# Performance work log

Hardware: AMD Instinct MI355X
Metric: run time of the kernel (lower is better)

## Reference

```python
import jax, jax.numpy as jnp
import numpy as np

NEG_SLOPE = 0.2

def gat_conv(x, src, dst, n, W, a_src, a_dst, b):
    # PyG GATConv, heads=1: h = xW; e_ij = LeakyReLU(a_src.h_j + a_dst.h_i)
    # alpha = softmax over incoming edges of i; out_i = sum_j alpha_ij * h_j + b
    h = x @ W                               # [N, F_out]
    s_src = h @ a_src                       # [N]
    s_dst = h @ a_dst                       # [N]
    e = s_src[src] + s_dst[dst]             # [E]
    e = jnp.where(e > 0, e, NEG_SLOPE * e)  # leaky relu
    # numerically stable scatter-softmax over destination groups
    m = jax.ops.segment_max(e, dst, num_segments=n)          # [N]
    ee = jnp.exp(e - m[dst])                                  # [E]
    denom = jax.ops.segment_sum(ee, dst, num_segments=n)      # [N]
    alpha = ee / denom[dst]                                    # [E]
    out = jax.ops.segment_sum(alpha[:, None] * h[src], dst, num_segments=n)
    return out + b

def add_self_loops(edge_index, n):
    loops = jnp.arange(n, dtype=edge_index.dtype)
    src = jnp.concatenate([edge_index[0], loops])
    dst = jnp.concatenate([edge_index[1], loops])
    return src, dst

def setup_inputs() -> dict:
    key = jax.random.key(0)
    ks = jax.random.split(key, 12)
    N, E, F_IN, H1, H2, C = 50000, 800000, 1433, 512, 256, 7
    x = jax.random.normal(ks[0], (N, F_IN), dtype=jnp.float32)
    edge_index = jax.random.randint(ks[1], (2, E), 0, N, dtype=jnp.int64)
    def glorot(k, shape):
        lim = float(np.sqrt(6.0 / (shape[0] + shape[-1])))
        return jax.random.uniform(k, shape, jnp.float32, -lim, lim)
    params = {
        'W1': glorot(ks[2], (F_IN, H1)), 'as1': glorot(ks[3], (H1,)), 'ad1': glorot(ks[4], (H1,)), 'b1': jnp.zeros((H1,), jnp.float32),
        'W2': glorot(ks[5], (H1, H2)), 'as2': glorot(ks[6], (H2,)), 'ad2': glorot(ks[7], (H2,)), 'b2': jnp.zeros((H2,), jnp.float32),
        'W3': glorot(ks[8], (H2, C)), 'as3': glorot(ks[9], (C,)), 'ad3': glorot(ks[10], (C,)), 'b3': jnp.zeros((C,), jnp.float32),
    }
    return {'x': x, 'edge_index': edge_index, **params}

def reference(x, edge_index, W1, as1, ad1, b1, W2, as2, ad2, b2, W3, as3, ad3, b3):
    n = x.shape[0]
    src, dst = add_self_loops(edge_index, n)
    h = jax.nn.relu(gat_conv(x, src, dst, n, W1, as1, ad1, b1))
    h = jax.nn.relu(gat_conv(h, src, dst, n, W2, as2, ad2, b2))
    h = gat_conv(h, src, dst, n, W3, as3, ad3, b3)
    return jax.nn.log_softmax(h, axis=1)
```

## Files before the change

### kernel.cpp

```cpp
#include <hip/hip_runtime.h>
#include <hip/hip_bf16.h>
#include <math.h>

constexpr int N_NODES = 50000;
constexpr int E_EDGES = 800000;
constexpr int E_TOT   = E_EDGES + N_NODES;
constexpr int F_IN  = 1433;
constexpr int KPAD1 = 1440;
constexpr int F1 = 512;
constexpr int F2 = 256;
constexpr int NC = 7;
constexpr int MAXDEG = 1024;
constexpr float NEG_SLOPE = 0.2f;

typedef unsigned short u16;
typedef unsigned int   u32;
typedef short s16x8 __attribute__((ext_vector_type(8)));
typedef u32   u32x4 __attribute__((ext_vector_type(4)));
typedef float f32x4 __attribute__((ext_vector_type(4)));

__device__ inline u16 f2b(float f) {
    u32 u = __float_as_uint(f);
    u32 r = (u + 0x7fffu + ((u >> 16) & 1u)) >> 16;
    return (u16)r;
}
__device__ inline float b2f(u16 b) { return __uint_as_float(((u32)b) << 16); }

__device__ inline u32 pkbf16(float lo, float hi) {
    union { __hip_bfloat162 h; u32 u; } c;
    c.h = __float22bfloat162_rn(make_float2(lo, hi));
    return c.u;
}

__device__ inline void gload_lds16(const void* g, void* l) {
    __builtin_amdgcn_global_load_lds(
        (const __attribute__((address_space(1))) u32*)g,
        (__attribute__((address_space(3))) u32*)l, 16, 0, 0);
}

__global__ void count_dst_kernel(const int* __restrict__ dst, int* __restrict__ counts) {
    int i = blockIdx.x * blockDim.x + threadIdx.x;
    if (i < E_TOT) {
        int d = (i < E_EDGES) ? dst[i] : (i - E_EDGES);
        atomicAdd(&counts[d], 1);
    }
}

__global__ __launch_bounds__(1024) void scan_kernel(const int* __restrict__ counts,
                                                    int* __restrict__ row_ptr, int n) {
    __shared__ int part[1024];
    int t = threadIdx.x;
    int chunk = (n + 1023) / 1024;
    int lo = t * chunk;
    int hi = min(lo + chunk, n);
    int s = 0;
    for (int i = lo; i < hi; ++i) s += counts[i];
    part[t] = s;
    __syncthreads();
    for (int off = 1; off < 1024; off <<= 1) {
        int v = 0;
        if (t >= off) v = part[t - off];
        __syncthreads();
        part[t] += v;
        __syncthreads();
    }
    int run = part[t] - s;
    for (int i = lo; i < hi; ++i) { row_ptr[i] = run; run += counts[i]; }
    if (t == 1023) row_ptr[n] = part[1023];
}

__global__ void scatter_kernel(const int* __restrict__ src, const int* __restrict__ dst,
                               const int* __restrict__ row_ptr, int* __restrict__ fill,
                               int* __restrict__ col) {
    int i = blockIdx.x * blockDim.x + threadIdx.x;
    if (i < E_TOT) {
        int s = (i < E_EDGES) ? src[i] : (i - E_EDGES);
        int d = (i < E_EDGES) ? dst[i] : (i - E_EDGES);
        int p = row_ptr[d] + atomicAdd(&fill[d], 1);
        col[p] = s;
    }
}

__global__ void convert_wt_kernel(const float* __restrict__ W, u32* __restrict__ Wt,
                                  int K, int Nn, int KP) {
    int p = blockIdx.x * blockDim.x + threadIdx.x;
    int ppr = KP / 2;
    if (p >= Nn * ppr) return;
    int n = p / ppr;
    int k = (p - n * ppr) * 2;
    float v0 = (k + 0 < K) ? W[(size_t)(k + 0) * Nn + n] : 0.f;
    float v1 = (k + 1 < K) ? W[(size_t)(k + 1) * Nn + n] : 0.f;
    Wt[p] = (u32)f2b(v0) | ((u32)f2b(v1) << 16);
}

__global__ __launch_bounds__(256) void mfma_gemm_xf32(const float* __restrict__ A,
                                                      const u16* __restrict__ Bt,
                                                      u16* __restrict__ C,
                                                      int M, int N, int Kf, int K32) {
    __shared__ float sA[128 * 32];
    __shared__ u16  sB[128 * 32];
    int tid  = threadIdx.x;
    int wave = tid >> 6;
    int lane = tid & 63;
    int quad = lane >> 4;
    int lm   = lane & 15;
    int wm = wave & 1;
    int wn = wave >> 1;
    int m0 = blockIdx.y * 128;
    int n0 = blockIdx.x * 128;

    int arow_sub = lane >> 3;
    int acol     = (lane & 7) * 4;
    int brow_sub = lane >> 2;
    int bcol     = (lane & 3) * 8;

    const float* gA[4];
    float* lA[4];
#pragma unroll
    for (int c = 0; c < 4; ++c) {
        int chunk = wave * 4 + c;
        int row = min(m0 + chunk * 8 + arow_sub, M - 1);
        gA[c] = A + (size_t)row * Kf + acol;
        lA[c] = &sA[chunk * 256];
    }
    const u16* gB[2];
    u16* lB[2];
#pragma unroll
    for (int c = 0; c < 2; ++c) {
        int chunk = wave * 2 + c;
        int row = n0 + chunk * 16 + brow_sub;
        gB[c] = Bt + (size_t)row * K32 + bcol;
        lB[c] = &sB[chunk * 512];
    }

    f32x4 acc[4][4];
#pragma unroll
    for (int i = 0; i < 4; ++i)
#pragma unroll
        for (int j = 0; j < 4; ++j) acc[i][j] = (f32x4){0.f, 0.f, 0.f, 0.f};

    int kLast = K32 - 32;
    for (int k0 = 0; k0 <= kLast; k0 += 32) {
        if (k0 < kLast) {
#pragma unroll
            for (int c = 0; c < 4; ++c) gload_lds16(gA[c] + k0, lA[c]);
        } else {
            int colc = min(k0 + acol, Kf - 4);
#pragma unroll
            for (int c = 0; c < 4; ++c) gload_lds16(gA[c] - acol + colc, lA[c]);
        }
#pragma unroll
        for (int c = 0; c < 2; ++c) gload_lds16(gB[c] + k0, lB[c]);
        __syncthreads();

        s16x8 af[4], bf[4];
#pragma unroll
        for (int mt = 0; mt < 4; ++mt) {
            const float* pa = &sA[(wm * 64 + mt * 16 + lm) * 32 + quad * 8];
            float4 u0 = *(const float4*)pa;
            float4 u1 = *(const float4*)(pa + 4);
            u32x4 aw;
            aw[0] = pkbf16(u0.x, u0.y);
            aw[1] = pkbf16(u0.z, u0.w);
            aw[2] = pkbf16(u1.x, u1.y);
            aw[3] = pkbf16(u1.z, u1.w);
            af[mt] = __builtin_bit_cast(s16x8, aw);
        }
#pragma unroll
        for (int nt = 0; nt < 4; ++nt)
            bf[nt] = *(const s16x8*)&sB[(wn * 64 + nt * 16 + lm) * 32 + quad * 8];
#pragma unroll
        for (int mt = 0; mt < 4; ++mt)
#pragma unroll
            for (int nt = 0; nt < 4; ++nt)
                acc[mt][nt] = __builtin_amdgcn_mfma_f32_16x16x32_bf16(
                    af[mt], bf[nt], acc[mt][nt], 0, 0, 0);
        __syncthreads();
    }

#pragma unroll
    for (int mt = 0; mt < 4; ++mt) {
        int mbase = m0 + wm * 64 + mt * 16 + quad * 4;
#pragma unroll
        for (int nt = 0; nt < 4; ++nt) {
            int n = n0 + wn * 64 + nt * 16 + lm;
#pragma unroll
            for (int r = 0; r < 4; ++r) {
                int m = mbase + r;
                if (m < M) C[(size_t)m * N + n] = f2b(acc[mt][nt][r]);
            }
        }
    }
}

__global__ __launch_bounds__(256) void mfma_gemm_bt(const u16* __restrict__ A,
                                                    const u16* __restrict__ Bt,
                                                    u16* __restrict__ C,
                                                    int M, int N, int K) {
    __shared__ u16 sA[128 * 32];
    __shared__ u16 sB[128 * 32];
    int tid  = threadIdx.x;
    int wave = tid >> 6;
    int lane = tid & 63;
    int quad = lane >> 4;
    int lm   = lane & 15;
    int wm = wave & 1;
    int wn = wave >> 1;
    int m0 = blockIdx.y * 128;
    int n0 = blockIdx.x * 128;

    int ch0 = wave * 2, ch1 = wave * 2 + 1;
    int rsub = lane >> 2;
    int csub = (lane & 3) * 8;
    int ar0 = min(m0 + ch0 * 16 + rsub, M - 1);
    int ar1 = min(m0 + ch1 * 16 + rsub, M - 1);
    int br0 = n0 + ch0 * 16 + rsub;
    int br1 = n0 + ch1 * 16 + rsub;
    const u16* gA0 = A + (size_t)ar0 * K + csub;
    const u16* gA1 = A + (size_t)ar1 * K + csub;
    const u16* gB0 = Bt + (size_t)br0 * K + csub;
    const u16* gB1 = Bt + (size_t)br1 * K + csub;

    f32x4 acc[4][4];
#pragma unroll
    for (int i = 0; i < 4; ++i)
#pragma unroll
        for (int j = 0; j < 4; ++j) acc[i][j] = (f32x4){0.f, 0.f, 0.f, 0.f};

    for (int k0 = 0; k0 < K; k0 += 32) {
        gload_lds16(gA0 + k0, &sA[ch0 * 512]);
        gload_lds16(gA1 + k0, &sA[ch1 * 512]);
        gload_lds16(gB0 + k0, &sB[ch0 * 512]);
        gload_lds16(gB1 + k0, &sB[ch1 * 512]);
        __syncthreads();

        s16x8 af[4], bf[4];
#pragma unroll
        for (int mt = 0; mt < 4; ++mt)
            af[mt] = *(const s16x8*)&sA[(wm * 64 + mt * 16 + lm) * 32 + quad * 8];
#pragma unroll
        for (int nt = 0; nt < 4; ++nt)
            bf[nt] = *(const s16x8*)&sB[(wn * 64 + nt * 16 + lm) * 32 + quad * 8];
#pragma unroll
        for (int mt = 0; mt < 4; ++mt)
#pragma unroll
            for (int nt = 0; nt < 4; ++nt)
                acc[mt][nt] = __builtin_amdgcn_mfma_f32_16x16x32_bf16(
                    af[mt], bf[nt], acc[mt][nt], 0, 0, 0);
        __syncthreads();
    }

#pragma unroll
    for (int mt = 0; mt < 4; ++mt) {
        int mbase = m0 + wm * 64 + mt * 16 + quad * 4;
#pragma unroll
        for (int nt = 0; nt < 4; ++nt) {
            int n = n0 + wn * 64 + nt * 16 + lm;
#pragma unroll
            for (int r = 0; r < 4; ++r) {
                int m = mbase + r;
                if (m < M) C[(size_t)m * N + n] = f2b(acc[mt][nt][r]);
            }
        }
    }
}

template <int F>
__global__ __launch_bounds__(256) void scores_bf16_kernel(const u16* __restrict__ h,
                                                          const float* __restrict__ a_src,
                                                          const float* __restrict__ a_dst,
                                                          float* __restrict__ s_src,
                                                          float* __restrict__ s_dst, int n) {
    int gwid = (blockIdx.x * blockDim.x + threadIdx.x) >> 6;
    int lane = threadIdx.x & 63;
    if (gwid >= n) return;
    const u32* row = (const u32*)(h + (size_t)gwid * F);
    float acc1 = 0.f, acc2 = 0.f;
    for (int p = lane; p < F / 2; p += 64) {
        u32 u = row[p];
        float v0 = b2f((u16)(u & 0xffff));
        float v1 = b2f((u16)(u >> 16));
        acc1 += v0 * a_src[2 * p] + v1 * a_src[2 * p + 1];
        acc2 += v0 * a_dst[2 * p] + v1 * a_dst[2 * p + 1];
    }
#pragma unroll
    for (int o = 32; o; o >>= 1) {
        acc1 += __shfl_xor(acc1, o);
        acc2 += __shfl_xor(acc2, o);
    }
    if (lane == 0) { s_src[gwid] = acc1; s_dst[gwid] = acc2; }
}

template <int F>
__global__ __launch_bounds__(256) void scores_kernel(const float* __restrict__ h,
                                                     const float* __restrict__ a_src,
                                                     const float* __restrict__ a_dst,
                                                     float* __restrict__ s_src,
                                                     float* __restrict__ s_dst, int n) {
    int gwid = (blockIdx.x * blockDim.x + threadIdx.x) >> 6;
    int lane = threadIdx.x & 63;
    if (gwid >= n) return;
    const float* row = h + (size_t)gwid * F;
    float acc1 = 0.f, acc2 = 0.f;
    for (int f = lane; f < F; f += 64) {
        float v = row[f];
        acc1 += v * a_src[f];
        acc2 += v * a_dst[f];
    }
#pragma unroll
    for (int o = 32; o; o >>= 1) {
        acc1 += __shfl_xor(acc1, o);
        acc2 += __shfl_xor(acc2, o);
    }
    if (lane == 0) { s_src[gwid] = acc1; s_dst[gwid] = acc2; }
}

template <int F, bool OUT_BF16>
__global__ __launch_bounds__(256) void agg_gather_kernel(const u16* __restrict__ h,
                                                         const float* __restrict__ s_src,
                                                         const float* __restrict__ s_dst,
                                                         const float* __restrict__ bias,
                                                         const int* __restrict__ row_ptr,
                                                         const int* __restrict__ col,
                                                         void* __restrict__ out) {
    constexpr int UPL = F / 128;
    int node = blockIdx.x;
    int tid = threadIdx.x;
    int wave = tid >> 6;
    int lane = tid & 63;
    int beg = row_ptr[node];
    int deg = min(row_ptr[node + 1] - beg, MAXDEG);

    __shared__ float w[MAXDEG];
    __shared__ int cs[MAXDEG];
    __shared__ float sdenom;
    __shared__ float red[4][F];

    if (wave == 0) {
        float sd = s_dst[node];
        float m = -1e30f;
        for (int j = lane; j < deg; j += 64) {
            int s = col[beg + j];
            cs[j] = s;
            float e = s_src[s] + sd;
            e = (e > 0.f) ? e : NEG_SLOPE * e;
            w[j] = e;
            m = fmaxf(m, e);
        }
#pragma unroll
        for (int o = 32; o; o >>= 1) m = fmaxf(m, __shfl_xor(m, o));
        float sum = 0.f;
        for (int j = lane; j < deg; j += 64) {
            float v = expf(w[j] - m);
            w[j] = v;
            sum += v;
        }
#pragma unroll
        for (int o = 32; o; o >>= 1) sum += __shfl_xor(sum, o);
        if (lane == 0) sdenom = sum;
    }
    __syncthreads();
    float inv = 1.0f / sdenom;

    float acc[2 * UPL];
#pragma unroll
    for (int e = 0; e < 2 * UPL; ++e) acc[e] = 0.f;

    int j = wave;
    for (; j + 4 < deg; j += 8) {
        float wg0 = w[j] * inv;
        float wg1 = w[j + 4] * inv;
        const u32* r0 = (const u32*)(h + (size_t)cs[j] * F) + lane * UPL;
        const u32* r1 = (const u32*)(h + (size_t)cs[j + 4] * F) + lane * UPL;
        u32 v0[UPL], v1[UPL];
        if constexpr (UPL == 4) {
            uint4 q0 = *(const uint4*)r0; v0[0] = q0.x; v0[1] = q0.y; v0[2] = q0.z; v0[3] = q0.w;
            uint4 q1 = *(const uint4*)r1; v1[0] = q1.x; v1[1] = q1.y; v1[2] = q1.z; v1[3] = q1.w;
        } else {
            uint2 q0 = *(const uint2*)r0; v0[0] = q0.x; v0[1] = q0.y;
            uint2 q1 = *(const uint2*)r1; v1[0] = q1.x; v1[1] = q1.y;
        }
#pragma unroll
        for (int u = 0; u < UPL; ++u) {
            acc[2 * u]     += wg0 * b2f((u16)(v0[u] & 0xffff)) + wg1 * b2f((u16)(v1[u] & 0xffff));
            acc[2 * u + 1] += wg0 * b2f((u16)(v0[u] >> 16))    + wg1 * b2f((u16)(v1[u] >> 16));
        }
    }
    if (j < deg) {
        float wg = w[j] * inv;
        const u32* r = (const u32*)(h + (size_t)cs[j] * F) + lane * UPL;
        u32 v[UPL];
        if constexpr (UPL == 4) {
            uint4 q = *(const uint4*)r; v[0] = q.x; v[1] = q.y; v[2] = q.z; v[3] = q.w;
        } else {
            uint2 q = *(const uint2*)r; v[0] = q.x; v[1] = q.y;
        }
#pragma unroll
        for (int u = 0; u < UPL; ++u) {
            acc[2 * u]     += wg * b2f((u16)(v[u] & 0xffff));
            acc[2 * u + 1] += wg * b2f((u16)(v[u] >> 16));
        }
    }

#pragma unroll
    for (int e = 0; e < 2 * UPL; ++e) red[wave][lane * 2 * UPL + e] = acc[e];
    __syncthreads();

    if constexpr (OUT_BF16) {
        if (tid < F / 2) {
            int f = tid * 2;
            float v0 = red[0][f] + red[1][f] + red[2][f] + red[3][f] + bias[f];
            float v1 = red[0][f + 1] + red[1][f + 1] + red[2][f + 1] + red[3][f + 1] + bias[f + 1];
            v0 = fmaxf(v0, 0.f);
            v1 = fmaxf(v1, 0.f);
            ((u32*)out)[(size_t)node * (F / 2) + tid] = (u32)f2b(v0) | ((u32)f2b(v1) << 16);
        }
    } else {
        if (tid < F) {
            float v = red[0][tid] + red[1][tid] + red[2][tid] + red[3][tid] + bias[tid];
            ((float*)out)[(size_t)node * F + tid] = fmaxf(v, 0.f);
        }
    }
}

__global__ __launch_bounds__(64) void agg_lsm7_kernel(const float* __restrict__ h,
                                                      const float* __restrict__ s_src,
                                                      const float* __restrict__ s_dst,
                                                      const float* __restrict__ bias,
                                                      const int* __restrict__ row_ptr,
                                                      const int* __restrict__ col,
                                                      float* __restrict__ out) {
    int node = blockIdx.x;
    int lane = threadIdx.x;
    int beg = row_ptr[node];
    int deg = min(row_ptr[node + 1] - beg, MAXDEG);

    __shared__ float w[MAXDEG];
    __shared__ int cs[MAXDEG];

    float sd = s_dst[node];
    float m = -1e30f;
    for (int j = lane; j < deg; j += 64) {
        int s = col[beg + j];
        cs[j] = s;
        float e = s_src[s] + sd;
        e = (e > 0.f) ? e : NEG_SLOPE * e;
        w[j] = e;
        m = fmaxf(m, e);
    }
#pragma unroll
    for (int o = 32; o; o >>= 1) m = fmaxf(m, __shfl_xor(m, o));
    float sum = 0.f;
    for (int j = lane; j < deg; j += 64) {
        float v = expf(w[j] - m);
        w[j] = v;
        sum += v;
    }
#pragma unroll
    for (int o = 32; o; o >>= 1) sum += __shfl_xor(sum, o);
    float inv = 1.0f / sum;

    float a[NC];
#pragma unroll
    for (int f = 0; f < NC; ++f) a[f] = 0.f;
    for (int j = lane; j < deg; j += 64) {
        float wg = w[j] * inv;
        const float* row = h + (size_t)cs[j] * NC;
#pragma unroll
        for (int f = 0; f < NC; ++f) a[f] += wg * row[f];
    }
#pragma unroll
    for (int f = 0; f < NC; ++f)
#pragma unroll
        for (int o = 32; o; o >>= 1) a[f] += __shfl_xor(a[f], o);

    if (lane == 0) {
        float vals[NC];
        float mx = -1e30f;
#pragma unroll
        for (int f = 0; f < NC; ++f) { vals[f] = a[f] + bias[f]; mx = fmaxf(mx, vals[f]); }
        float ssum = 0.f;
#pragma unroll
        for (int f = 0; f < NC; ++f) ssum += expf(vals[f] - mx);
        float lse = mx + logf(ssum);
#pragma unroll
        for (int f = 0; f < NC; ++f) out[(size_t)node * NC + f] = vals[f] - lse;
    }
}

__global__ __launch_bounds__(256) void gemm3_kernel(const float* __restrict__ A,
                                                    const float* __restrict__ W,
                                                    float* __restrict__ out, int n) {
    __shared__ float sW[F2 * NC];
    for (int i = threadIdx.x; i < F2 * NC; i += blockDim.x) sW[i] = W[i];
    __syncthreads();
    int gwid = (blockIdx.x * blockDim.x + threadIdx.x) >> 6;
    int lane = threadIdx.x & 63;
    if (gwid >= n) return;
    const float* row = A + (size_t)gwid * F2;
    float4 v = *(const float4*)(row + lane * 4);
    float res = 0.f;
#pragma unroll
    for (int c = 0; c < NC; ++c) {
        float p = v.x * sW[(lane * 4 + 0) * NC + c] + v.y * sW[(lane * 4 + 1) * NC + c] +
                  v.z * sW[(lane * 4 + 2) * NC + c] + v.w * sW[(lane * 4 + 3) * NC + c];
#pragma unroll
        for (int o = 32; o; o >>= 1) p += __shfl_xor(p, o);
        if (lane == c) res = p;
    }
    if (lane < NC) out[(size_t)gwid * NC + lane] = res;
}

extern "C" void kernel_launch(void* const* d_in, const int* in_sizes, int n_in,
                              void* d_out, int out_size, void* d_ws, size_t ws_size,
                              hipStream_t stream) {
    const float* x   = (const float*)d_in[0];
    const int* ei    = (const int*)d_in[1];
    const int* src   = ei;
    const int* dst   = ei + E_EDGES;
    const float* W1  = (const float*)d_in[2];
    const float* as1 = (const float*)d_in[3];
    const float* ad1 = (const float*)d_in[4];
    const float* b1  = (const float*)d_in[5];
    const float* W2  = (const float*)d_in[6];
    const float* as2 = (const float*)d_in[7];
    const float* ad2 = (const float*)d_in[8];
    const float* b2  = (const float*)d_in[9];
    const float* W3  = (const float*)d_in[10];
    const float* as3 = (const float*)d_in[11];
    const float* ad3 = (const float*)d_in[12];
    const float* b3  = (const float*)d_in[13];
    float* outp = (float*)d_out;

    char* base = (char*)d_ws;
    u16*  a1b = (u16*)base;
    u16*  h2b = (u16*)(base + 51200000);
    float* a2 = (float*)(base + 76800000);
    float* h3 = (float*)(base + 128000000);
    u16*  h1b = (u16*)(base + 144000000);
    u16*  W1t = (u16*)(base + 195200000);
    u16*  W2t = (u16*)(base + 196674560);
    float* ssrc = (float*)(base + 196936704);
    float* sdst = (float*)(base + 197136704);
    int* row_ptr = (int*)(base + 197336704);
    int* counts  = (int*)(base + 197536708);
    int* fill    = (int*)(base + 197736708);
    int* col     = (int*)(base + 197936708);

    hipMemsetAsync(counts, 0, sizeof(int) * N_NODES, stream);
    hipMemsetAsync(fill, 0, sizeof(int) * N_NODES, stream);

    {
        int blk = 256;
        int grid = (E_TOT + blk - 1) / blk;
        count_dst_kernel<<<grid, blk, 0, stream>>>(dst, counts);
        scan_kernel<<<1, 1024, 0, stream>>>(counts, row_ptr, N_NODES);
        scatter_kernel<<<grid, blk, 0, stream>>>(src, dst, row_ptr, fill, col);
    }

    {
        int nw1 = F1 * (KPAD1 / 2);
        convert_wt_kernel<<<(nw1 + 255) / 256, 256, 0, stream>>>(W1, (u32*)W1t, F_IN, F1, KPAD1);
        int nw2 = F2 * (F1 / 2);
        convert_wt_kernel<<<(nw2 + 255) / 256, 256, 0, stream>>>(W2, (u32*)W2t, F1, F2, F1);
    }

    int waves_grid = (N_NODES + 3) / 4;
    int mblocks = (N_NODES + 127) / 128;

    {
        dim3 grid(F1 / 128, mblocks);
        mfma_gemm_xf32<<<grid, 256, 0, stream>>>(x, W1t, h1b, N_NODES, F1, F_IN, KPAD1);
        scores_bf16_kernel<F1><<<waves_grid, 256, 0, stream>>>(h1b, as1, ad1, ssrc, sdst, N_NODES);
        agg_gather_kernel<F1, true><<<N_NODES, 256, 0, stream>>>(
            h1b, ssrc, sdst, b1, row_ptr, col, a1b);
    }
    {
        dim3 grid(F2 / 128, mblocks);
        mfma_gemm_bt<<<grid, 256, 0, stream>>>(a1b, W2t, h2b, N_NODES, F2, F1);
        scores_bf16_kernel<F2><<<waves_grid, 256, 0, stream>>>(h2b, as2, ad2, ssrc, sdst, N_NODES);
        agg_gather_kernel<F2, false><<<N_NODES, 256, 0, stream>>>(
            h2b, ssrc, sdst, b2, row_ptr, col, a2);
    }
    {
        gemm3_kernel<<<waves_grid, 256, 0, stream>>>(a2, W3, h3, N_NODES);
        scores_kernel<NC><<<waves_grid, 256, 0, stream>>>(h3, as3, ad3, ssrc, sdst, N_NODES);
        agg_lsm7_kernel<<<N_NODES, 64, 0, stream>>>(
            h3, ssrc, sdst, b3, row_ptr, col, outp);
    }
}
```

Baseline: 1.117 ms.

## Restructure layer-1 GEMM to 64x512 tiles so x is read once

Layer 1's GEMM now uses 64-row by full-512-column tiles instead of 128x128. Each block reads its rows of fp32 x exactly once, rather than once per each of the four column blocks. The fp32-to-bf16 conversion of A is done once per tile into a separate LDS buffer, not per wave in registers, and the ragged K tail gets its own guarded scalar-load path. This cuts redundant global traffic on the large fp32 input. The cost is 32 accumulators per wave, a much larger B tile in LDS, an extra barrier per K step, and fewer rows per block.

```diff
diff --git a/kernel.cpp b/kernel.cpp
--- a/kernel.cpp
+++ b/kernel.cpp
@@ -16,7 +16,6 @@
 typedef unsigned short u16;
 typedef unsigned int   u32;
 typedef short s16x8 __attribute__((ext_vector_type(8)));
-typedef u32   u32x4 __attribute__((ext_vector_type(4)));
 typedef float f32x4 __attribute__((ext_vector_type(4)));
 
 __device__ inline u16 f2b(float f) {
@@ -93,101 +92,118 @@
     Wt[p] = (u32)f2b(v0) | ((u32)f2b(v1) << 16);
 }
 
-__global__ __launch_bounds__(256) void mfma_gemm_xf32(const float* __restrict__ A,
+__global__ __launch_bounds__(256, 2) void gemm1_fused(const float* __restrict__ A,
                                                       const u16* __restrict__ Bt,
-                                                      u16* __restrict__ C,
-                                                      int M, int N, int Kf, int K32) {
-    __shared__ float sA[128 * 32];
-    __shared__ u16  sB[128 * 32];
+                                                      u16* __restrict__ C) {
+    constexpr int M = N_NODES;
+    __shared__ float sA32[64 * 32];
+    __shared__ u16  sAb[64 * 32];
+    __shared__ u16  sB[512 * 32];
     int tid  = threadIdx.x;
     int wave = tid >> 6;
     int lane = tid & 63;
     int quad = lane >> 4;
     int lm   = lane & 15;
-    int wm = wave & 1;
-    int wn = wave >> 1;
-    int m0 = blockIdx.y * 128;
-    int n0 = blockIdx.x * 128;
-
-    int arow_sub = lane >> 3;
-    int acol     = (lane & 7) * 4;
-    int brow_sub = lane >> 2;
-    int bcol     = (lane & 3) * 8;
-
-    const float* gA[4];
-    float* lA[4];
-#pragma unroll
-    for (int c = 0; c < 4; ++c) {
-        int chunk = wave * 4 + c;
-        int row = min(m0 + chunk * 8 + arow_sub, M - 1);
-        gA[c] = A + (size_t)row * Kf + acol;
-        lA[c] = &sA[chunk * 256];
-    }
-    const u16* gB[2];
-    u16* lB[2];
+    int m0 = blockIdx.x * 64;
+
+    const float* gA[2];
+    float* lA[2];
 #pragma unroll
     for (int c = 0; c < 2; ++c) {
         int chunk = wave * 2 + c;
-        int row = n0 + chunk * 16 + brow_sub;
-        gB[c] = Bt + (size_t)row * K32 + bcol;
+        int row = min(m0 + chunk * 8 + (lane >> 3), M - 1);
+        gA[c] = A + (size_t)row * F_IN + (lane & 7) * 4;
+        lA[c] = &sA32[chunk * 256];
+    }
+    const u16* gB[8];
+    u16* lB[8];
+#pragma unroll
+    for (int c = 0; c < 8; ++c) {
+        int chunk = wave * 8 + c;
+        int row = chunk * 16 + (lane >> 2);
+        gB[c] = Bt + (size_t)row * KPAD1 + (lane & 3) * 8;
         lB[c] = &sB[chunk * 512];
     }
 
-    f32x4 acc[4][4];
+    f32x4 acc[4][8];
 #pragma unroll
     for (int i = 0; i < 4; ++i)
 #pragma unroll
-        for (int j = 0; j < 4; ++j) acc[i][j] = (f32x4){0.f, 0.f, 0.f, 0.f};
-
-    int kLast = K32 - 32;
-    for (int k0 = 0; k0 <= kLast; k0 += 32) {
-        if (k0 < kLast) {
-#pragma unroll
-            for (int c = 0; c < 4; ++c) gload_lds16(gA[c] + k0, lA[c]);
-        } else {
-            int colc = min(k0 + acol, Kf - 4);
-#pragma unroll
-            for (int c = 0; c < 4; ++c) gload_lds16(gA[c] - acol + colc, lA[c]);
-        }
-#pragma unroll
-        for (int c = 0; c < 2; ++c) gload_lds16(gB[c] + k0, lB[c]);
-        __syncthreads();
-
-        s16x8 af[4], bf[4];
-#pragma unroll
-        for (int mt = 0; mt < 4; ++mt) {
-            const float* pa = &sA[(wm * 64 + mt * 16 + lm) * 32 + quad * 8];
-            float4 u0 = *(const float4*)pa;
-            float4 u1 = *(const float4*)(pa + 4);
-            u32x4 aw;
-            aw[0] = pkbf16(u0.x, u0.y);
-            aw[1] = pkbf16(u0.z, u0.w);
-            aw[2] = pkbf16(u1.x, u1.y);
-            aw[3] = pkbf16(u1.z, u1.w);
-            af[mt] = __builtin_bit_cast(s16x8, aw);
-        }
-#pragma unroll
-        for (int nt = 0; nt < 4; ++nt)
-            bf[nt] = *(const s16x8*)&sB[(wn * 64 + nt * 16 + lm) * 32 + quad * 8];
+        for (int j = 0; j < 8; ++j) acc[i][j] = (f32x4){0.f, 0.f, 0.f, 0.f};
+
+    constexpr int K_MAIN = 1408;
+    for (int k0 = 0; k0 < K_MAIN; k0 += 32) {
+#pragma unroll
+        for (int c = 0; c < 2; ++c) gload_lds16(gA[c] + k0, lA[c]);
+#pragma unroll
+        for (int c = 0; c < 8; ++c) gload_lds16(gB[c] + k0, lB[c]);
+        __syncthreads();
+
+#pragma unroll
+        for (int j = 0; j < 4; ++j) {
+            float2 v = *(const float2*)&sA32[2 * tid + 512 * j];
+            ((u32*)sAb)[tid + 256 * j] = pkbf16(v.x, v.y);
+        }
+        __syncthreads();
+
+        s16x8 af[4], bf[8];
 #pragma unroll
         for (int mt = 0; mt < 4; ++mt)
-#pragma unroll
-            for (int nt = 0; nt < 4; ++nt)
+            af[mt] = *(const s16x8*)&sAb[(mt * 16 + lm) * 32 + quad * 8];
+#pragma unroll
+        for (int nt = 0; nt < 8; ++nt)
+            bf[nt] = *(const s16x8*)&sB[(wave * 128 + nt * 16 + lm) * 32 + quad * 8];
+#pragma unroll
+        for (int mt = 0; mt < 4; ++mt)
+#pragma unroll
+            for (int nt = 0; nt < 8; ++nt)
                 acc[mt][nt] = __builtin_amdgcn_mfma_f32_16x16x32_bf16(
                     af[mt], bf[nt], acc[mt][nt], 0, 0, 0);
         __syncthreads();
     }
 
+    {
+        constexpr int k0 = K_MAIN;
+#pragma unroll
+        for (int c = 0; c < 8; ++c) gload_lds16(gB[c] + k0, lB[c]);
+#pragma unroll
+        for (int j = 0; j < 4; ++j) {
+            int s = 2 * tid + 512 * j;
+            int row = s >> 5;
+            int gk = k0 + (s & 31);
+            int ar = min(m0 + row, M - 1);
+            const float* xr = A + (size_t)ar * F_IN;
+            float v0 = (gk + 0 < F_IN) ? xr[gk + 0] : 0.f;
+            float v1 = (gk + 1 < F_IN) ? xr[gk + 1] : 0.f;
+            ((u32*)sAb)[tid + 256 * j] = pkbf16(v0, v1);
+        }
+        __syncthreads();
+
+        s16x8 af[4], bf[8];
+#pragma unroll
+        for (int mt = 0; mt < 4; ++mt)
+            af[mt] = *(const s16x8*)&sAb[(mt * 16 + lm) * 32 + quad * 8];
+#pragma unroll
+        for (int nt = 0; nt < 8; ++nt)
+            bf[nt] = *(const s16x8*)&sB[(wave * 128 + nt * 16 + lm) * 32 + quad * 8];
+#pragma unroll
+        for (int mt = 0; mt < 4; ++mt)
+#pragma unroll
+            for (int nt = 0; nt < 8; ++nt)
+                acc[mt][nt] = __builtin_amdgcn_mfma_f32_16x16x32_bf16(
+                    af[mt], bf[nt], acc[mt][nt], 0, 0, 0);
+    }
+
 #pragma unroll
     for (int mt = 0; mt < 4; ++mt) {
-        int mbase = m0 + wm * 64 + mt * 16 + quad * 4;
-#pragma unroll
-        for (int nt = 0; nt < 4; ++nt) {
-            int n = n0 + wn * 64 + nt * 16 + lm;
+        int mbase = m0 + mt * 16 + quad * 4;
+#pragma unroll
+        for (int nt = 0; nt < 8; ++nt) {
+            int n = wave * 128 + nt * 16 + lm;
 #pragma unroll
             for (int r = 0; r < 4; ++r) {
                 int m = mbase + r;
-                if (m < M) C[(size_t)m * N + n] = f2b(acc[mt][nt][r]);
+                if (m < M) C[(size_t)m * F1 + n] = f2b(acc[mt][nt][r]);
             }
         }
     }
@@ -569,8 +585,8 @@
     int mblocks = (N_NODES + 127) / 128;
 
     {
-        dim3 grid(F1 / 128, mblocks);
-        mfma_gemm_xf32<<<grid, 256, 0, stream>>>(x, W1t, h1b, N_NODES, F1, F_IN, KPAD1);
+        int grid1 = (N_NODES + 63) / 64;
+        gemm1_fused<<<grid1, 256, 0, stream>>>(x, W1t, h1b);
         scores_bf16_kernel<F1><<<waves_grid, 256, 0, stream>>>(h1b, as1, ad1, ssrc, sdst, N_NODES);
         agg_gather_kernel<F1, true><<<N_NODES, 256, 0, stream>>>(
             h1b, ssrc, sdst, b1, row_ptr, col, a1b);
```

New measurement: 1.086 ms. -2.8%, faster.
